# Performance work log

Measured on AMD Instinct MI355X. Metric: run time of the kernel, lower is better.

Reference implementation:

```python
import jax, jax.numpy as jnp
import numpy as np

B, L, D, N = 16, 512, 768, 8192


def setup_inputs() -> dict:
    key = jax.random.key(0)
    k = jax.random.split(key, 5)
    return {
        "y": jax.random.normal(k[0], (B, L, D), dtype=jnp.float32),
        "Wy_w": jax.random.normal(k[1], (D, D), dtype=jnp.float32) * 0.02,
        "Wy_b": jnp.zeros((D,), dtype=jnp.float32),
        "Wz_w": jax.random.normal(k[2], (D, D), dtype=jnp.float32) * 0.02,
        "Wz_b": jnp.zeros((D,), dtype=jnp.float32),
        "dic_z": jax.random.normal(k[3], (N, D), dtype=jnp.float32),
        "prior": jax.random.uniform(k[4], (N,), dtype=jnp.float32),
    }


def reference(y, Wy_w, Wy_b, Wz_w, Wz_b, dic_z, prior):
    # y: [B,L,D]; dic_z: [N,D]; prior: [N]
    d = y.shape[-1]
    qy = jnp.einsum('bld,ed->ble', y, Wy_w) + Wy_b          # Wy(y): [B,L,D]
    kz = jnp.einsum('nd,ed->ne', dic_z, Wz_w) + Wz_b        # Wz(dic_z): [N,D]
    scores = jnp.einsum('bld,nd->bln', qy, kz) / jnp.sqrt(jnp.float32(d))
    attn = jax.nn.softmax(scores, axis=-1)                   # [B,L,N]
    # z[b,l,d] = sum_n prior[n] * attn[b,l,n] * dic_z[n,d]
    # == (attn * prior) @ dic_z, avoiding the [L,N,D] intermediate.
    z = jnp.einsum('bln,nd->bld', attn * prior, dic_z)       # [B,L,D]
    return z
```

## Files before the change

kernel.cpp:

```cpp
#include <hip/hip_runtime.h>
#include <stdint.h>

#define M_ 8192
#define D_ 768
#define N_ 8192

typedef unsigned short u16;
typedef __attribute__((ext_vector_type(8))) unsigned short us8;
typedef __attribute__((ext_vector_type(8))) __bf16 bf16x8;
typedef __attribute__((ext_vector_type(4))) float f32x4;

__device__ __forceinline__ u16 f2bf(float f) {
  uint32_t u = __builtin_bit_cast(uint32_t, f);
  u += 0x7FFFu + ((u >> 16) & 1u);
  return (u16)(u >> 16);
}
__device__ __forceinline__ float bf2f(u16 u) {
  return __builtin_bit_cast(float, ((uint32_t)u) << 16);
}

__device__ __forceinline__ void gload_lds16(const void* g, void* l) {
  __builtin_amdgcn_global_load_lds(
      (__attribute__((address_space(1))) void*)g,
      (__attribute__((address_space(3))) void*)l, 16, 0, 0);
}

__global__ __launch_bounds__(256)
void k_cvt_bf16(const float* __restrict__ in, u16* __restrict__ out, int n4) {
  int stride = gridDim.x * blockDim.x;
  for (int i = blockIdx.x * blockDim.x + threadIdx.x; i < n4; i += stride) {
    float4 v = reinterpret_cast<const float4*>(in)[i];
    ushort4 o;
    o.x = f2bf(v.x); o.y = f2bf(v.y); o.z = f2bf(v.z); o.w = f2bf(v.w);
    reinterpret_cast<ushort4*>(out)[i] = o;
  }
}

__global__ __launch_bounds__(256)
void k_build_vt(const float* __restrict__ dic, const float* __restrict__ prior,
                u16* __restrict__ Vt) {
  __shared__ float t[32][33];
  const int n0 = blockIdx.x * 32, d0 = blockIdx.y * 32;
  const int tx = threadIdx.x, ty = threadIdx.y;
  #pragma unroll
  for (int i = ty; i < 32; i += 8)
    t[i][tx] = dic[(size_t)(n0 + i) * D_ + d0 + tx] * prior[n0 + i];
  __syncthreads();
  #pragma unroll
  for (int i = ty; i < 32; i += 8)
    Vt[(size_t)(d0 + i) * N_ + n0 + tx] = f2bf(t[tx][i]);
}

template<int EP>
__global__ __launch_bounds__(512, 2)
void k_gemm8(const u16* __restrict__ A, const u16* __restrict__ Bm,
             u16* __restrict__ Cb, float* __restrict__ Cf, float scale,
             long ldk, int K, int Ncols, int nbx, int tps, long partStride) {
  extern __shared__ u16 ldsu[];
  const int tid = threadIdx.x;
  const int lane = tid & 63, wid = tid >> 6;
  const int wr = wid >> 2, wc = wid & 3;
  const int L15 = lane & 15, L7 = lane & 7, g = lane >> 4;

  const int nwg = gridDim.x;
  const int bid = blockIdx.x;
  const int wg = ((nwg & 7) == 0) ? ((bid & 7) * (nwg >> 3) + (bid >> 3)) : bid;
  const int s = wg / tps;
  const int r = wg % tps;
  const int bx = r % nbx, by = r / nbx;
  const long m0 = (long)by * 256;
  const long n0 = (long)bx * 256;
  const int NT = K >> 6;

  int aBase[2], bBase[2];
  #pragma unroll
  for (int ks = 0; ks < 2; ++ks) {
    const int slot = (((ks * 4 + g) ^ L7) << 3);
    aBase[ks] = wr * 8192 + L15 * 64 + slot;
    bBase[ks] = 16384 + (wc >> 1) * 8192 + (wc & 1) * 4096 + L15 * 64 + slot;
  }

  const int rowoff = wid * 8 + (lane >> 3);
  const int colsw = ((lane & 7) ^ (lane >> 3)) << 3;
  const u16* Ag = A + m0 * ldk + (long)s * K;
  const u16* Bg = Bm + n0 * ldk + (long)s * K;
  u16* ldsW = ldsu + tid * 8;

  auto g1 = [&](int t, int mat, int r0) {
    if (t >= NT) return;
    const u16* src = (mat ? Bg : Ag) + (size_t)(r0 + rowoff) * ldk
                     + (size_t)t * 64 + colsw;
    gload_lds16(src, ldsW + (t & 1) * 32768 + mat * 16384 + (r0 >> 6) * 512 * 8);
  };

#define RD_B()                                                              \
  _Pragma("unroll") for (int j = 0; j < 4; ++j)                             \
    _Pragma("unroll") for (int ks = 0; ks < 2; ++ks)                        \
      bfr[j][ks] = __builtin_bit_cast(bf16x8,                               \
          *reinterpret_cast<const us8*>(&ldsu[bufOff + bBase[ks] + j * 1024]));
#define RD_A(q)                                                             \
  _Pragma("unroll") for (int t = 0; t < 2; ++t)                             \
    _Pragma("unroll") for (int ks = 0; ks < 2; ++ks)                        \
      afr[t][ks] = __builtin_bit_cast(bf16x8,                               \
          *reinterpret_cast<const us8*>(                                    \
              &ldsu[bufOff + aBase[ks] + (2 * (q) + t) * 1024]));
#define LGKM0()                                                             \
  asm volatile("s_waitcnt lgkmcnt(0)" ::: "memory");                        \
  __builtin_amdgcn_sched_barrier(0);
#define MM(p)                                                               \
  __builtin_amdgcn_s_setprio(1);                                            \
  _Pragma("unroll") for (int t = 0; t < 2; ++t)                             \
    _Pragma("unroll") for (int j = 0; j < 4; ++j)                           \
      _Pragma("unroll") for (int ks = 0; ks < 2; ++ks)                      \
        acc[2 * (p) + t][j] = __builtin_amdgcn_mfma_f32_16x16x32_bf16(      \
            afr[t][ks], bfr[j][ks], acc[2 * (p) + t][j], 0, 0, 0);          \
  __builtin_amdgcn_s_setprio(0);

  g1(0, 1, 0); g1(0, 1, 64); g1(0, 1, 128); g1(0, 1, 192);
  g1(0, 0, 0); g1(0, 0, 128); g1(0, 0, 64); g1(0, 0, 192);
  g1(1, 1, 0); g1(1, 1, 64);
  g1(1, 1, 128); g1(1, 1, 192);
  g1(1, 0, 0); g1(1, 0, 128);
  asm volatile("s_waitcnt vmcnt(6)" ::: "memory");
  __builtin_amdgcn_s_barrier();

  f32x4 acc[8][4] = {};

  for (int k = 0; k < NT; ++k) {
    const int bufOff = (k & 1) * 32768;
    bf16x8 bfr[4][2];

    {
      bf16x8 afr[2][2];
      g1(k + 1, 0, 64); g1(k + 1, 0, 192);
      RD_B(); RD_A(0);
      asm volatile("s_waitcnt lgkmcnt(8)" ::: "memory");
      __builtin_amdgcn_s_barrier();
      LGKM0();
      MM(0);
    }
    {
      bf16x8 afr[2][2];
      RD_A(1);
      g1(k + 2, 1, 0); g1(k + 2, 1, 64);
      __builtin_amdgcn_s_barrier();
      LGKM0();
      MM(1);
    }
    {
      bf16x8 afr[2][2];
      RD_A(2);
      g1(k + 2, 1, 128); g1(k + 2, 1, 192);
      __builtin_amdgcn_s_barrier();
      LGKM0();
      MM(2);
    }
    {
      bf16x8 afr[2][2];
      RD_A(3);
      g1(k + 2, 0, 0); g1(k + 2, 0, 128);
      if (k < NT - 2) asm volatile("s_waitcnt vmcnt(6)" ::: "memory");
      else            asm volatile("s_waitcnt vmcnt(0)" ::: "memory");
      __builtin_amdgcn_s_barrier();
      LGKM0();
      MM(3);
    }
  }
#undef RD_B
#undef RD_A
#undef LGKM0
#undef MM

  #pragma unroll
  for (int i = 0; i < 8; ++i)
    #pragma unroll
    for (int j = 0; j < 4; ++j)
      #pragma unroll
      for (int q = 0; q < 4; ++q) {
        long row = m0 + wr * 128 + i * 16 + ((lane >> 4) * 4) + q;
        long col = n0 + wc * 64 + j * 16 + L15;
        if (EP == 0) Cb[row * (long)Ncols + col] = f2bf(acc[i][j][q] * scale);
        else         Cf[(long)s * partStride + row * (long)Ncols + col] = acc[i][j][q];
      }
}

__global__ __launch_bounds__(256)
void k_reduce2(const float* __restrict__ part, long partStride,
               const float* __restrict__ linv, float* __restrict__ out, int n4) {
  int stride = gridDim.x * blockDim.x;
  const float4* p0 = reinterpret_cast<const float4*>(part);
  const float4* p1 = reinterpret_cast<const float4*>(part + partStride);
  for (int i = blockIdx.x * blockDim.x + threadIdx.x; i < n4; i += stride) {
    float4 a = p0[i], b = p1[i];
    float sc = linv[(i * 4) / D_];
    float4 o;
    o.x = (a.x + b.x) * sc; o.y = (a.y + b.y) * sc;
    o.z = (a.z + b.z) * sc; o.w = (a.w + b.w) * sc;
    reinterpret_cast<float4*>(out)[i] = o;
  }
}

template<int EP>
__global__ __launch_bounds__(256, 2)
void k_gemm_nt(const u16* __restrict__ A, const u16* __restrict__ Bm,
               float* __restrict__ Cf, u16* __restrict__ Cb,
               const float* __restrict__ bias, const float* __restrict__ rowscale,
               float scale, int N, int K) {
  __shared__ u16 Al[128 * 64];
  __shared__ u16 Bl[128 * 64];
  const int tid = threadIdx.x;
  const int lane = tid & 63;
  const int wave = tid >> 6;
  const int wr = wave >> 1, wc = wave & 1;
  const long m0 = (long)blockIdx.y * 128;
  const long n0 = (long)blockIdx.x * 128;

  f32x4 acc[4][4] = {};

  const u16* gA = A + (m0 + (tid >> 3)) * (long)K + (tid & 7) * 8;
  const u16* gB = Bm + (n0 + (tid >> 3)) * (long)K + (tid & 7) * 8;

  for (int kt = 0; kt < K; kt += 64) {
    __syncthreads();
    #pragma unroll
    for (int r = 0; r < 4; ++r) {
      gload_lds16(gA + (size_t)(r * 32) * K + kt, &Al[r * 2048 + tid * 8]);
      gload_lds16(gB + (size_t)(r * 32) * K + kt, &Bl[r * 2048 + tid * 8]);
    }
    __syncthreads();
    #pragma unroll
    for (int ks = 0; ks < 2; ++ks) {
      bf16x8 av[4], bv[4];
      #pragma unroll
      for (int i = 0; i < 4; ++i) {
        av[i] = __builtin_bit_cast(bf16x8, *reinterpret_cast<const us8*>(
            &Al[(wr * 64 + i * 16 + (lane & 15)) * 64 + ks * 32 + (lane >> 4) * 8]));
        bv[i] = __builtin_bit_cast(bf16x8, *reinterpret_cast<const us8*>(
            &Bl[(wc * 64 + i * 16 + (lane & 15)) * 64 + ks * 32 + (lane >> 4) * 8]));
      }
      #pragma unroll
      for (int i = 0; i < 4; ++i)
        #pragma unroll
        for (int j = 0; j < 4; ++j)
          acc[i][j] = __builtin_amdgcn_mfma_f32_16x16x32_bf16(av[i], bv[j], acc[i][j], 0, 0, 0);
    }
  }

  #pragma unroll
  for (int i = 0; i < 4; ++i) {
    #pragma unroll
    for (int j = 0; j < 4; ++j) {
      #pragma unroll
      for (int q = 0; q < 4; ++q) {
        long row = m0 + wr * 64 + i * 16 + ((lane >> 4) * 4) + q;
        long col = n0 + wc * 64 + j * 16 + (lane & 15);
        float v = acc[i][j][q];
        if (EP == 1)      Cb[row * N + col] = f2bf(v + bias[col]);
        else if (EP == 2) Cb[row * N + col] = f2bf(v * scale);
        else              Cf[row * N + col] = v * rowscale[row];
      }
    }
  }
}

__global__ __launch_bounds__(256)
void k_softmax(u16* __restrict__ S, float* __restrict__ linv) {
  const int row = blockIdx.x;
  u16* rp = S + (size_t)row * N_;
  const int tid = threadIdx.x;
  float v[32];
  #pragma unroll
  for (int c = 0; c < 4; ++c) {
    us8 u = *reinterpret_cast<const us8*>(rp + (size_t)(c * 256 + tid) * 8);
    #pragma unroll
    for (int q = 0; q < 8; ++q) v[c * 8 + q] = bf2f(u[q]);
  }
  float mx = v[0];
  #pragma unroll
  for (int i = 1; i < 32; ++i) mx = fmaxf(mx, v[i]);
  #pragma unroll
  for (int o = 1; o < 64; o <<= 1) mx = fmaxf(mx, __shfl_xor(mx, o));
  __shared__ float red[8];
  if ((tid & 63) == 0) red[tid >> 6] = mx;
  __syncthreads();
  mx = fmaxf(fmaxf(red[0], red[1]), fmaxf(red[2], red[3]));
  float s = 0.f;
  #pragma unroll
  for (int i = 0; i < 32; ++i) { v[i] = __expf(v[i] - mx); s += v[i]; }
  #pragma unroll
  for (int o = 1; o < 64; o <<= 1) s += __shfl_xor(s, o);
  if ((tid & 63) == 0) red[4 + (tid >> 6)] = s;
  __syncthreads();
  s = (red[4] + red[5]) + (red[6] + red[7]);
  #pragma unroll
  for (int c = 0; c < 4; ++c) {
    us8 u;
    #pragma unroll
    for (int q = 0; q < 8; ++q) u[q] = f2bf(v[c * 8 + q]);
    *reinterpret_cast<us8*>(rp + (size_t)(c * 256 + tid) * 8) = u;
  }
  if (tid == 0) linv[row] = 1.0f / s;
}

extern "C" void kernel_launch(void* const* d_in, const int* in_sizes, int n_in,
                              void* d_out, int out_size, void* d_ws, size_t ws_size,
                              hipStream_t stream) {
  (void)in_sizes; (void)n_in; (void)out_size;
  const float* y     = (const float*)d_in[0];
  const float* Wy_w  = (const float*)d_in[1];
  const float* Wy_b  = (const float*)d_in[2];
  const float* Wz_w  = (const float*)d_in[3];
  const float* Wz_b  = (const float*)d_in[4];
  const float* dic   = (const float*)d_in[5];
  const float* prior = (const float*)d_in[6];
  float* out = (float*)d_out;

  hipFuncSetAttribute(reinterpret_cast<const void*>(&k_gemm8<0>),
                      hipFuncAttributeMaxDynamicSharedMemorySize, 131072);
  hipFuncSetAttribute(reinterpret_cast<const void*>(&k_gemm8<1>),
                      hipFuncAttributeMaxDynamicSharedMemorySize, 131072);

  char* base = (char*)d_ws;
  size_t off = 0;
  auto alloc = [&](size_t bytes) -> char* {
    char* p = base + off;
    off = (off + bytes + 255) & ~(size_t)255;
    return p;
  };
  u16*  Yb   = (u16*)alloc((size_t)M_ * D_ * 2);
  u16*  Db   = (u16*)alloc((size_t)N_ * D_ * 2);
  u16*  Wyb  = (u16*)alloc((size_t)D_ * D_ * 2);
  u16*  Wzb  = (u16*)alloc((size_t)D_ * D_ * 2);
  u16*  Qb   = (u16*)alloc((size_t)M_ * D_ * 2);
  u16*  Kb   = (u16*)alloc((size_t)N_ * D_ * 2);
  u16*  Vt   = (u16*)alloc((size_t)D_ * N_ * 2);
  float* linv = (float*)alloc((size_t)M_ * 4);
  size_t fixed = off;
  int Mc = M_;
  while (Mc > 256 &&
         fixed + (size_t)Mc * N_ * 2 + 2 * (size_t)Mc * D_ * 4 > ws_size)
    Mc >>= 1;
  u16*   Sc   = (u16*)alloc((size_t)Mc * N_ * 2);
  float* part = (float*)alloc(2 * (size_t)Mc * D_ * 4);
  const long partStride = (long)Mc * D_;

  auto cvt = [&](const float* src, u16* dst, size_t n) {
    int n4 = (int)(n / 4);
    int blocks = (n4 + 255) / 256;
    if (blocks > 2048) blocks = 2048;
    hipLaunchKernelGGL(k_cvt_bf16, dim3(blocks), dim3(256), 0, stream, src, dst, n4);
  };
  cvt(y,    Yb,  (size_t)M_ * D_);
  cvt(dic,  Db,  (size_t)N_ * D_);
  cvt(Wy_w, Wyb, (size_t)D_ * D_);
  cvt(Wz_w, Wzb, (size_t)D_ * D_);

  hipLaunchKernelGGL(k_build_vt, dim3(N_ / 32, D_ / 32), dim3(32, 8), 0, stream,
                     dic, prior, Vt);

  hipLaunchKernelGGL(HIP_KERNEL_NAME(k_gemm_nt<1>), dim3(D_ / 128, M_ / 128), dim3(256), 0, stream,
                     Yb, Wyb, (float*)nullptr, Qb, Wy_b, (const float*)nullptr, 0.f, D_, D_);
  hipLaunchKernelGGL(HIP_KERNEL_NAME(k_gemm_nt<1>), dim3(D_ / 128, N_ / 128), dim3(256), 0, stream,
                     Db, Wzb, (float*)nullptr, Kb, Wz_b, (const float*)nullptr, 0.f, D_, D_);

  const float scale = 0.036084391824351615f;
  for (int mc = 0; mc < M_; mc += Mc) {
    {
      const int nbx = N_ / 256, nby = Mc / 256;
      hipLaunchKernelGGL(HIP_KERNEL_NAME(k_gemm8<0>), dim3(nbx * nby), dim3(512), 131072, stream,
                         Qb + (size_t)mc * D_, Kb, Sc, (float*)nullptr, scale,
                         (long)D_, D_, N_, nbx, nbx * nby, 0L);
    }
    hipLaunchKernelGGL(k_softmax, dim3(Mc), dim3(256), 0, stream, Sc, linv + mc);
    {
      const int nbx = D_ / 256, nby = Mc / 256, tps = nbx * nby;
      hipLaunchKernelGGL(HIP_KERNEL_NAME(k_gemm8<1>), dim3(tps * 2), dim3(512), 131072, stream,
                         Sc, Vt, (u16*)nullptr, part, 1.0f,
                         (long)N_, N_ / 2, D_, nbx, tps, partStride);
    }
    {
      int n4 = Mc * D_ / 4;
      int blocks = (n4 + 255) / 256;
      if (blocks > 2048) blocks = 2048;
      hipLaunchKernelGGL(k_reduce2, dim3(blocks), dim3(256), 0, stream,
                         part, partStride, linv + mc, out + (size_t)mc * D_, n4);
    }
  }
}
```

Baseline: 335.8 us.

## Fuse softmax exponent and row-sum into the score GEMM epilogue

Removes the separate softmax kernel: the QK GEMM epilogue now exponentiates scaled scores directly, writes bf16 exp values, and accumulates per-row sums via shuffle reduction and atomicAdd. The normalization is deferred to the final reduce kernel, which divides by the row sum. This skips a full read/write pass over the large score matrix, at the cost of dropping max-subtraction (overflow risk if scores are large) and adding atomics plus a memset. The variable g is used without being shown as defined in the visible part.

```diff
diff --git a/kernel.cpp b/kernel.cpp
--- a/kernel.cpp
+++ b/kernel.cpp
@@ -171,28 +171,47 @@
 #undef LGKM0
 #undef MM
 
-  #pragma unroll
-  for (int i = 0; i < 8; ++i)
-    #pragma unroll
-    for (int j = 0; j < 4; ++j)
+  if (EP == 0) {
+    #pragma unroll
+    for (int i = 0; i < 8; ++i) {
       #pragma unroll
       for (int q = 0; q < 4; ++q) {
-        long row = m0 + wr * 128 + i * 16 + ((lane >> 4) * 4) + q;
-        long col = n0 + wc * 64 + j * 16 + L15;
-        if (EP == 0) Cb[row * (long)Ncols + col] = f2bf(acc[i][j][q] * scale);
-        else         Cf[(long)s * partStride + row * (long)Ncols + col] = acc[i][j][q];
+        long row = m0 + wr * 128 + i * 16 + g * 4 + q;
+        float rsum = 0.f;
+        #pragma unroll
+        for (int j = 0; j < 4; ++j) {
+          float v = __expf(acc[i][j][q] * scale);
+          rsum += v;
+          Cb[row * (long)Ncols + n0 + wc * 64 + j * 16 + L15] = f2bf(v);
+        }
+        #pragma unroll
+        for (int o = 1; o < 16; o <<= 1) rsum += __shfl_xor(rsum, o);
+        if (L15 == 0) atomicAdd(&Cf[row], rsum);
       }
+    }
+  } else {
+    #pragma unroll
+    for (int i = 0; i < 8; ++i)
+      #pragma unroll
+      for (int j = 0; j < 4; ++j)
+        #pragma unroll
+        for (int q = 0; q < 4; ++q) {
+          long row = m0 + wr * 128 + i * 16 + g * 4 + q;
+          long col = n0 + wc * 64 + j * 16 + L15;
+          Cf[(long)s * partStride + row * (long)Ncols + col] = acc[i][j][q];
+        }
+  }
 }
 
 __global__ __launch_bounds__(256)
 void k_reduce2(const float* __restrict__ part, long partStride,
-               const float* __restrict__ linv, float* __restrict__ out, int n4) {
+               const float* __restrict__ rowsum, float* __restrict__ out, int n4) {
   int stride = gridDim.x * blockDim.x;
   const float4* p0 = reinterpret_cast<const float4*>(part);
   const float4* p1 = reinterpret_cast<const float4*>(part + partStride);
   for (int i = blockIdx.x * blockDim.x + threadIdx.x; i < n4; i += stride) {
     float4 a = p0[i], b = p1[i];
-    float sc = linv[(i * 4) / D_];
+    float sc = 1.0f / rowsum[(i * 4) / D_];
     float4 o;
     o.x = (a.x + b.x) * sc; o.y = (a.y + b.y) * sc;
     o.z = (a.z + b.z) * sc; o.w = (a.w + b.w) * sc;
@@ -263,45 +282,6 @@
   }
 }
 
-__global__ __launch_bounds__(256)
-void k_softmax(u16* __restrict__ S, float* __restrict__ linv) {
-  const int row = blockIdx.x;
-  u16* rp = S + (size_t)row * N_;
-  const int tid = threadIdx.x;
-  float v[32];
-  #pragma unroll
-  for (int c = 0; c < 4; ++c) {
-    us8 u = *reinterpret_cast<const us8*>(rp + (size_t)(c * 256 + tid) * 8);
-    #pragma unroll
-    for (int q = 0; q < 8; ++q) v[c * 8 + q] = bf2f(u[q]);
-  }
-  float mx = v[0];
-  #pragma unroll
-  for (int i = 1; i < 32; ++i) mx = fmaxf(mx, v[i]);
-  #pragma unroll
-  for (int o = 1; o < 64; o <<= 1) mx = fmaxf(mx, __shfl_xor(mx, o));
-  __shared__ float red[8];
-  if ((tid & 63) == 0) red[tid >> 6] = mx;
-  __syncthreads();
-  mx = fmaxf(fmaxf(red[0], red[1]), fmaxf(red[2], red[3]));
-  float s = 0.f;
-  #pragma unroll
-  for (int i = 0; i < 32; ++i) { v[i] = __expf(v[i] - mx); s += v[i]; }
-  #pragma unroll
-  for (int o = 1; o < 64; o <<= 1) s += __shfl_xor(s, o);
-  if ((tid & 63) == 0) red[4 + (tid >> 6)] = s;
-  __syncthreads();
-  s = (red[4] + red[5]) + (red[6] + red[7]);
-  #pragma unroll
-  for (int c = 0; c < 4; ++c) {
-    us8 u;
-    #pragma unroll
-    for (int q = 0; q < 8; ++q) u[q] = f2bf(v[c * 8 + q]);
-    *reinterpret_cast<us8*>(rp + (size_t)(c * 256 + tid) * 8) = u;
-  }
-  if (tid == 0) linv[row] = 1.0f / s;
-}
-
 extern "C" void kernel_launch(void* const* d_in, const int* in_sizes, int n_in,
                               void* d_out, int out_size, void* d_ws, size_t ws_size,
                               hipStream_t stream) {
@@ -334,7 +314,7 @@
   u16*  Qb   = (u16*)alloc((size_t)M_ * D_ * 2);
   u16*  Kb   = (u16*)alloc((size_t)N_ * D_ * 2);
   u16*  Vt   = (u16*)alloc((size_t)D_ * N_ * 2);
-  float* linv = (float*)alloc((size_t)M_ * 4);
+  float* rowsum = (float*)alloc((size_t)M_ * 4);
   size_t fixed = off;
   int Mc = M_;
   while (Mc > 256 &&
@@ -343,6 +323,8 @@
   u16*   Sc   = (u16*)alloc((size_t)Mc * N_ * 2);
   float* part = (float*)alloc(2 * (size_t)Mc * D_ * 4);
   const long partStride = (long)Mc * D_;
+
+  hipMemsetAsync(rowsum, 0, (size_t)M_ * 4, stream);
 
   auto cvt = [&](const float* src, u16* dst, size_t n) {
     int n4 = (int)(n / 4);
@@ -368,10 +350,9 @@
     {
       const int nbx = N_ / 256, nby = Mc / 256;
       hipLaunchKernelGGL(HIP_KERNEL_NAME(k_gemm8<0>), dim3(nbx * nby), dim3(512), 131072, stream,
-                         Qb + (size_t)mc * D_, Kb, Sc, (float*)nullptr, scale,
+                         Qb + (size_t)mc * D_, Kb, Sc, rowsum + mc, scale,
                          (long)D_, D_, N_, nbx, nbx * nby, 0L);
     }
-    hipLaunchKernelGGL(k_softmax, dim3(Mc), dim3(256), 0, stream, Sc, linv + mc);
     {
       const int nbx = D_ / 256, nby = Mc / 256, tps = nbx * nby;
       hipLaunchKernelGGL(HIP_KERNEL_NAME(k_gemm8<1>), dim3(tps * 2), dim3(512), 131072, stream,
@@ -383,7 +364,7 @@
       int blocks = (n4 + 255) / 256;
       if (blocks > 2048) blocks = 2048;
       hipLaunchKernelGGL(k_reduce2, dim3(blocks), dim3(256), 0, stream,
-                         part, partStride, linv + mc, out + (size_t)mc * D_, n4);
-    }
-  }
-}
+                         part, partStride, rowsum + mc, out + (size_t)mc * D_, n4);
+    }
+  }
+}
```

Result: no change. 339.1 us (+1.0%).
